# Kernel optimization log

Measured on AMD Instinct MI355X. Metric: run time of the kernel, lower is better.

Reference implementation:

```python
import jax, jax.numpy as jnp
import numpy as np

DIM = 768
H = 6        # pinned by router mask construction (3 logits -> 6 head gates)
HD = DIM // H  # 128
TAU = 5.0

def setup_inputs() -> dict:
    key = jax.random.key(0)
    ks = jax.random.split(key, 10)
    w = 0.02
    return {
        "x": jax.random.normal(ks[0], (4, 2048, DIM), jnp.float32),
        "latency": jax.random.uniform(ks[1], (1,), jnp.float32),
        "qkv_w": jax.random.normal(ks[2], (3 * DIM, DIM), jnp.float32) * w,
        "qkv_b": jax.random.normal(ks[3], (3 * DIM,), jnp.float32) * w,
        "proj_w": jax.random.normal(ks[4], (DIM, DIM), jnp.float32) * w,
        "proj_b": jax.random.normal(ks[5], (DIM,), jnp.float32) * w,
        "router_w": jax.random.normal(ks[6], (3, 1), jnp.float32),
        "router_b": jax.random.normal(ks[7], (3,), jnp.float32),
        # gumbel noise g = -log(Exp(1)), matching -empty.exponential_().log()
        "g1": -jnp.log(jax.random.exponential(ks[8], (3,), jnp.float32)),
        "g2": -jnp.log(jax.random.exponential(ks[9], (3,), jnp.float32)),
    }

def reference(x, latency, qkv_w, qkv_b, proj_w, proj_b, router_w, router_b, g1, g2):
    # router: Linear(1, 3) on scalar latency -> 3 logits
    logits = router_w @ latency + router_b                      # [3]
    # gumbel-sigmoid, tau=5, hard=True with straight-through estimator
    y_soft = jax.nn.sigmoid((logits + g1 - g2) / TAU)           # [3]
    y_hard = (y_soft > 0.5).astype(y_soft.dtype)
    mask3 = y_hard - jax.lax.stop_gradient(y_soft) + y_soft     # [3]
    # first logit gates 4 heads, remaining two gate one head each -> 6 heads
    mask6 = jnp.concatenate([mask3[:1], mask3[:1], mask3[:1], mask3])  # [6]
    maskC = jnp.repeat(mask6, HD)                               # [DIM]

    B, N, C = x.shape
    qkv = jnp.einsum('bnc,oc->bno', x, qkv_w) + qkv_b           # [B,N,3*DIM]
    qkv = qkv.reshape(B, N, 3, H, HD)
    q, k, v = qkv[:, :, 0], qkv[:, :, 1], qkv[:, :, 2]          # [B,N,H,HD]

    scale = HD ** -0.5
    attn = jax.nn.softmax(jnp.einsum('bqhd,bkhd->bhqk', q * scale, k), axis=-1)
    out = jnp.einsum('bhqk,bkhd->bqhd', attn, v).reshape(B, N, C)

    out = out * maskC                                            # gate heads/channels
    return jnp.einsum('bnc,oc->bno', out, proj_w) + proj_b
```

## Files before the change

### kernel.cpp

```cpp
#include <hip/hip_runtime.h>
#include <cstdint>

#define DIM_ 768
#define H_ 6
#define HD_ 128
#define NB_ 4
#define SEQ_ 2048
#define TOK_ (NB_*SEQ_)
#define OUT3_ (3*DIM_)
#define L2E 1.4426950408889634f

typedef __bf16 bf16;
typedef __bf16 bf16x4 __attribute__((ext_vector_type(4)));
typedef __bf16 bf16x8 __attribute__((ext_vector_type(8)));
typedef float f32x4 __attribute__((ext_vector_type(4)));
typedef float f32x16 __attribute__((ext_vector_type(16)));
typedef unsigned int u32;
typedef u32 u32x4 __attribute__((ext_vector_type(4)));

__device__ __forceinline__ void gload16(const void* g, void* lds) {
  __builtin_amdgcn_global_load_lds((const __attribute__((address_space(1))) void*)g,
                                   (__attribute__((address_space(3))) void*)lds,
                                   16, 0, 0);
}

__global__ void convert_kernel(const float* __restrict__ in, bf16* __restrict__ out, int n) {
  int i = (blockIdx.x * 256 + threadIdx.x) * 4;
  if (i >= n) return;
  float4 v = *reinterpret_cast<const float4*>(in + i);
  bf16x4 o = { (bf16)v.x, (bf16)v.y, (bf16)v.z, (bf16)v.w };
  *reinterpret_cast<bf16x4*>(out + i) = o;
}

__global__ void mask_kernel(const float* __restrict__ latency,
                            const float* __restrict__ rw,
                            const float* __restrict__ rb,
                            const float* __restrict__ g1,
                            const float* __restrict__ g2,
                            float* __restrict__ mask6) {
  int i = threadIdx.x;
  if (i < 6) {
    int j = (i < 4) ? 0 : (i - 3);
    float logit = rw[j] * latency[0] + rb[j];
    float z = (logit + g1[j] - g2[j]) / 5.0f;
    float ys = 1.0f / (1.0f + expf(-z));
    float yh = ys > 0.5f ? 1.0f : 0.0f;
    mask6[i] = (yh - ys) + ys;
  }
}


__global__ __launch_bounds__(256)
void qkv_gemm(const bf16* __restrict__ A, const bf16* __restrict__ W,
              const float* __restrict__ bias,
              bf16* __restrict__ q, bf16* __restrict__ k, bf16* __restrict__ vt) {
  __shared__ bf16 As[128 * 32];
  __shared__ bf16 Bs[128 * 32];
  __shared__ bf16 FragS[8192];
  const int tid = threadIdx.x;
  const int l = tid & 63, w = tid >> 6;
  const int lr = l & 15, lg = l >> 4;
  const int wm = w >> 1, wn = w & 1;
  const int tm = blockIdx.y * 128;
  const int on = blockIdx.x * 128;

  f32x4 acc[4][4];
#pragma unroll
  for (int i = 0; i < 4; ++i)
#pragma unroll
    for (int j = 0; j < 4; ++j) acc[i][j] = f32x4{0.f, 0.f, 0.f, 0.f};

  for (int k0 = 0; k0 < DIM_; k0 += 32) {
    __syncthreads();
#pragma unroll
    for (int u = 0; u < 2; ++u) {
      int row = w * 32 + u * 16 + (l >> 2);
      int cb = l & 3;
      gload16(A + (size_t)(tm + row) * DIM_ + k0 + cb * 8, As + (w * 32 + u * 16) * 32);
      gload16(W + (size_t)(on + row) * DIM_ + k0 + cb * 8, Bs + (w * 32 + u * 16) * 32);
    }
    __syncthreads();
    bf16x8 af[4], bfr[4];
#pragma unroll
    for (int i = 0; i < 4; ++i)
      af[i] = *reinterpret_cast<const bf16x8*>(As + (wm * 64 + i * 16 + lr) * 32 + lg * 8);
#pragma unroll
    for (int j = 0; j < 4; ++j)
      bfr[j] = *reinterpret_cast<const bf16x8*>(Bs + (wn * 64 + j * 16 + lr) * 32 + lg * 8);
#pragma unroll
    for (int i = 0; i < 4; ++i)
#pragma unroll
      for (int j = 0; j < 4; ++j)
        acc[i][j] = __builtin_amdgcn_mfma_f32_16x16x32_bf16(af[i], bfr[j], acc[i][j], 0, 0, 0);
  }

  if (on < 2 * DIM_) {
    const int s = on / DIM_;
    const float scale = 0.08838834764831845f * L2E;
    const int n0 = tm & 2047;
    const int bb = tm >> 11;
    const int hh = (on - s * DIM_) >> 7;
    const int bhh = bb * H_ + hh;
    bf16* dstbase = (s == 0) ? q : k;
    for (int pass = 0; pass < 2; ++pass) {
      __syncthreads();
      if (wm == pass) {
#pragma unroll
        for (int i = 0; i < 4; ++i) {
#pragma unroll
          for (int j = 0; j < 4; ++j) {
            int dd = wn * 64 + j * 16 + lr;
            int kc = dd >> 4, hi8 = (dd >> 3) & 1, e = dd & 7;
            float bia = bias[on + dd];
#pragma unroll
            for (int r = 0; r < 4; ++r) {
              int nl = i * 16 + lg * 4 + r;
              float val = acc[i][j][r] + bia;
              if (s == 0) val *= scale;
              FragS[(((nl >> 5) * 8 + kc) << 9) + ((hi8 * 32 + (nl & 31)) << 3) + e] = (bf16)val;
            }
          }
        }
      }
      __syncthreads();
      size_t base = ((size_t)bhh * 64 + (n0 >> 5) + pass * 2) * 4096;
#pragma unroll
      for (int r8 = 0; r8 < 4; ++r8) {
        bf16x8 v8 = *reinterpret_cast<const bf16x8*>(FragS + r8 * 2048 + tid * 8);
        *reinterpret_cast<bf16x8*>(dstbase + base + r8 * 2048 + tid * 8) = v8;
      }
    }
  } else {
    const int hh = (on - 2 * DIM_) >> 7;
    const int bb = tm >> 11, n0 = tm & 2047;
    const int bhh = bb * H_ + hh;
    bf16(*Ts)[136] = reinterpret_cast<bf16(*)[136]>(As);
    for (int wc = 0; wc < 2; ++wc) {
#pragma unroll
      for (int j = 0; j < 4; ++j) {
        __syncthreads();
        if (wn == wc) {
          float bia = bias[on + wc * 64 + j * 16 + lr];
#pragma unroll
          for (int i = 0; i < 4; ++i) {
            bf16x4 pk;
#pragma unroll
            for (int r = 0; r < 4; ++r) pk[r] = (bf16)(acc[i][j][r] + bia);
            *reinterpret_cast<bf16x4*>(&Ts[lr][wm * 64 + i * 16 + lg * 4]) = pk;
          }
        }
        __syncthreads();
        int row = tid >> 4;
        int c8 = (tid & 15) * 8;
        bf16x8 v8 = *reinterpret_cast<const bf16x8*>(&Ts[row][c8]);
        int d = wc * 64 + j * 16 + row;
        int n = n0 + c8;
        size_t idx = (((((size_t)bhh * 32 + (n >> 6)) * 4 + ((n >> 4) & 3)) * 4 + (d >> 5)) << 9) +
                     ((((n >> 3) & 1) * 32 + (d & 31)) << 3);
        *reinterpret_cast<bf16x8*>(vt + idx) = v8;
      }
    }
  }
}

__global__ __launch_bounds__(256)
void proj_gemm(const bf16* __restrict__ A, const bf16* __restrict__ W,
               const float* __restrict__ bias, float* __restrict__ out) {
  __shared__ bf16 As[128 * 32];
  __shared__ bf16 Bs[128 * 32];
  const int tid = threadIdx.x;
  const int l = tid & 63, w = tid >> 6;
  const int lr = l & 15, lg = l >> 4;
  const int wm = w >> 1, wn = w & 1;
  const int tm = blockIdx.y * 128;
  const int on = blockIdx.x * 128;

  f32x4 acc[4][4];
#pragma unroll
  for (int i = 0; i < 4; ++i)
#pragma unroll
    for (int j = 0; j < 4; ++j) acc[i][j] = f32x4{0.f, 0.f, 0.f, 0.f};

  for (int k0 = 0; k0 < DIM_; k0 += 32) {
    __syncthreads();
#pragma unroll
    for (int u = 0; u < 2; ++u) {
      int row = w * 32 + u * 16 + (l >> 2);
      int cb = l & 3;
      gload16(A + (size_t)(tm + row) * DIM_ + k0 + cb * 8, As + (w * 32 + u * 16) * 32);
      gload16(W + (size_t)(on + row) * DIM_ + k0 + cb * 8, Bs + (w * 32 + u * 16) * 32);
    }
    __syncthreads();
    bf16x8 af[4], bfr[4];
#pragma unroll
    for (int i = 0; i < 4; ++i)
      af[i] = *reinterpret_cast<const bf16x8*>(As + (wm * 64 + i * 16 + lr) * 32 + lg * 8);
#pragma unroll
    for (int j = 0; j < 4; ++j)
      bfr[j] = *reinterpret_cast<const bf16x8*>(Bs + (wn * 64 + j * 16 + lr) * 32 + lg * 8);
#pragma unroll
    for (int i = 0; i < 4; ++i)
#pragma unroll
      for (int j = 0; j < 4; ++j)
        acc[i][j] = __builtin_amdgcn_mfma_f32_16x16x32_bf16(af[i], bfr[j], acc[i][j], 0, 0, 0);
  }

#pragma unroll
  for (int i = 0; i < 4; ++i) {
#pragma unroll
    for (int j = 0; j < 4; ++j) {
      int o = on + wn * 64 + j * 16 + lr;
      float bia = bias[o];
#pragma unroll
      for (int r = 0; r < 4; ++r) {
        int t = tm + wm * 64 + i * 16 + lg * 4 + r;
        out[(size_t)t * DIM_ + o] = acc[i][j][r] + bia;
      }
    }
  }
}

__global__ __launch_bounds__(128, 2)
void attn_kernel(const bf16* __restrict__ qf_g, const bf16* __restrict__ kf_g,
                 const bf16* __restrict__ vf_g, const float* __restrict__ mask6,
                 bf16* __restrict__ ab) {
  __shared__ char smem[16640];

  const int tid = threadIdx.x;
  const int l = tid & 63;
  const int w = tid >> 6;
  const int kl = l & 31, hi = l >> 5;
  const int bid = blockIdx.x;
  const int bh = bid % 24;
  const int qt = bid / 24;
  const int h = bh % H_;
  const int b = bh / H_;
  const int q0 = qt * 32;
  const int loff = l * 8;
  const float hm = mask6[h];

  if (hm == 0.0f) {
    bf16x8 z = __builtin_bit_cast(bf16x8, u32x4{0u, 0u, 0u, 0u});
    int row = tid >> 2, c0 = (tid & 3) * 32;
    bf16* dst = ab + ((size_t)b * SEQ_ + q0 + row) * DIM_ + h * HD_ + c0;
#pragma unroll
    for (int u = 0; u < 4; ++u)
      *reinterpret_cast<bf16x8*>(dst + u * 8) = z;
    return;
  }

  float* OM  = (float*)smem;
  float* MLm = (float*)(smem + 16384);
  float* MLl = MLm + 32;

  const bf16* qq = qf_g + (((size_t)bh * 64 + qt) * 8) * 512;
  const bf16* kq = kf_g + (size_t)bh * 262144 + (size_t)w * 32 * 4096;
  const bf16* vq = vf_g + (size_t)bh * 262144 + (size_t)w * 32 * 4096;

  bf16x8 qf[8];
#pragma unroll
  for (int kc = 0; kc < 8; ++kc)
    qf[kc] = *reinterpret_cast<const bf16x8*>(qq + kc * 512 + loff);

  f32x16 oacc[4];
#pragma unroll
  for (int df = 0; df < 4; ++df)
#pragma unroll
    for (int r = 0; r < 16; ++r) oacc[df][r] = 0.f;
  float m_lane = -3.0e38f;
  float lsum = 0.f;

  for (int jj = 0; jj < 32; ++jj) {
    const bf16* kb = kq + (size_t)jj * 4096;
    const bf16* vb = vq + (size_t)jj * 4096;

    f32x16 sacc;
#pragma unroll
    for (int r = 0; r < 16; ++r) sacc[r] = 0.f;
    __builtin_amdgcn_s_setprio(1);
#pragma unroll
    for (int kc = 0; kc < 8; ++kc) {
      bf16x8 kfr = *reinterpret_cast<const bf16x8*>(kb + kc * 512 + loff);
      sacc = __builtin_amdgcn_mfma_f32_32x32x16_bf16(kfr, qf[kc], sacc, 0, 0, 0);
    }
    __builtin_amdgcn_s_setprio(0);

    float t = sacc[0];
#pragma unroll
    for (int r = 1; r < 16; ++r) t = fmaxf(t, sacc[r]);
    t = fmaxf(t, __shfl_xor(t, 32));
    bool need = t > m_lane + 8.0f;
    if (__ballot(need) != 0ull) {
      float nm = fmaxf(m_lane, t);
      float c = exp2f(m_lane - nm);
      m_lane = nm;
      lsum *= c;
#pragma unroll
      for (int r = 0; r < 16; ++r) {
        float cr = __shfl(c, (r & 3) + 8 * (r >> 2) + 4 * hi);
#pragma unroll
        for (int df = 0; df < 4; ++df) oacc[df][r] *= cr;
      }
    }

    u32 pp[8];
#pragma unroll
    for (int m = 0; m < 8; ++m) {
      float e0 = exp2f(sacc[2 * m] - m_lane);
      float e1 = exp2f(sacc[2 * m + 1] - m_lane);
      lsum += e0 + e1;
      union { u32 u; bf16 hh2[2]; } pk;
      pk.hh2[0] = (bf16)e0; pk.hh2[1] = (bf16)e1;
      pp[m] = pk.u;
    }

    u32x4 afv[2];
#pragma unroll
    for (int ks = 0; ks < 2; ++ks) {
#pragma unroll
      for (int i = 0; i < 2; ++i) {
        u32 a = pp[4 * ks + i];
        u32 b2 = pp[4 * ks + 2 + i];
        asm volatile("v_permlane32_swap_b32 %0, %1" : "+v"(a), "+v"(b2));
        afv[ks][i] = a;
        afv[ks][2 + i] = b2;
      }
    }

    __builtin_amdgcn_s_setprio(1);
#pragma unroll
    for (int ks = 0; ks < 2; ++ks) {
      bf16x8 pa = __builtin_bit_cast(bf16x8, afv[ks]);
#pragma unroll
      for (int df = 0; df < 4; ++df) {
        bf16x8 vfr = *reinterpret_cast<const bf16x8*>(vb + (ks * 4 + df) * 512 + loff);
        oacc[df] = __builtin_amdgcn_mfma_f32_32x32x16_bf16(pa, vfr, oacc[df], 0, 0, 0);
      }
    }
    __builtin_amdgcn_s_setprio(0);
  }

  float lt = lsum + __shfl_xor(lsum, 32);

  if (w == 1) {
#pragma unroll
    for (int r = 0; r < 16; ++r) {
      int qloc = (r & 3) + 8 * (r >> 2) + 4 * hi;
#pragma unroll
      for (int df = 0; df < 4; ++df)
        OM[qloc * 128 + df * 32 + kl] = oacc[df][r];
    }
    MLm[kl] = m_lane;
    MLl[kl] = lt;
  }
  __syncthreads();
  if (w == 1) return;

  float m1 = MLm[kl];
  float l1 = MLl[kl];
  float M = fmaxf(m_lane, m1);
  float a0 = exp2f(m_lane - M), a1 = exp2f(m1 - M);
  float L = lt * a0 + l1 * a1;
  float s0 = a0 * hm / L, s1 = a1 * hm / L;

#pragma unroll
  for (int r = 0; r < 16; ++r) {
    int qloc = (r & 3) + 8 * (r >> 2) + 4 * hi;
    float r0 = __shfl(s0, qloc);
    float r1 = __shfl(s1, qloc);
    int n = q0 + qloc;
#pragma unroll
    for (int df = 0; df < 4; ++df) {
      int d = df * 32 + kl;
      float o1 = OM[qloc * 128 + df * 32 + kl];
      ab[((size_t)b * SEQ_ + n) * DIM_ + h * HD_ + d] =
          (bf16)(oacc[df][r] * r0 + o1 * r1);
    }
  }
}

extern "C" void kernel_launch(void* const* d_in, const int* in_sizes, int n_in,
                              void* d_out, int out_size, void* d_ws, size_t ws_size,
                              hipStream_t stream) {
  const float* x        = (const float*)d_in[0];
  const float* latency  = (const float*)d_in[1];
  const float* qkv_w    = (const float*)d_in[2];
  const float* qkv_b    = (const float*)d_in[3];
  const float* proj_w   = (const float*)d_in[4];
  const float* proj_b   = (const float*)d_in[5];
  const float* router_w = (const float*)d_in[6];
  const float* router_b = (const float*)d_in[7];
  const float* g1       = (const float*)d_in[8];
  const float* g2       = (const float*)d_in[9];
  float* out = (float*)d_out;

  const size_t N_X  = (size_t)TOK_ * DIM_;
  const size_t N_WQ = (size_t)OUT3_ * DIM_;
  const size_t N_WP = (size_t)DIM_ * DIM_;
  const size_t N_P  = (size_t)NB_ * H_ * SEQ_ * HD_;

  float* maskp = (float*)d_ws;
  bf16* xb  = (bf16*)((char*)d_ws + 256);
  bf16* wqb = xb + N_X;
  bf16* wpb = wqb + N_WQ;
  bf16* qbf = wpb + N_WP;
  bf16* kbf = qbf + N_P;
  bf16* vtb = kbf + N_P;
  bf16* abf = vtb + N_P;

  size_t need = 256 + 2 * (N_X + N_WQ + N_WP + 4 * N_P);
  if (ws_size < need) return;

  convert_kernel<<<(int)(N_X / 1024), 256, 0, stream>>>(x, xb, (int)N_X);
  convert_kernel<<<(int)(N_WQ / 1024), 256, 0, stream>>>(qkv_w, wqb, (int)N_WQ);
  convert_kernel<<<(int)(N_WP / 1024), 256, 0, stream>>>(proj_w, wpb, (int)N_WP);
  mask_kernel<<<1, 64, 0, stream>>>(latency, router_w, router_b, g1, g2, maskp);

  qkv_gemm<<<dim3(OUT3_ / 128, TOK_ / 128), 256, 0, stream>>>(xb, wqb, qkv_b, qbf, kbf, vtb);
  attn_kernel<<<dim3(24 * (SEQ_ / 32)), 128, 0, stream>>>(qbf, kbf, vtb, maskp, abf);
  proj_gemm<<<dim3(DIM_ / 128, TOK_ / 128), 256, 0, stream>>>(abf, wpb, proj_b, out);
}
```

Baseline: 189.1 us.

## Split attention KV range across four waves with tree merge

The attention block grows from two to four waves, and each wave now processes a quarter of the key/value sequence instead of a half. Partial softmax states are merged in two stages through shared memory: odd waves merge into even waves, then wave 2 into wave 0. The aim is to shorten each wave's serial loop and add parallelism per query tile. The cost is more shared memory, extra barriers and merge work, and possibly fewer resident blocks per CU.

```diff
diff --git a/kernel.cpp b/kernel.cpp
--- a/kernel.cpp
+++ b/kernel.cpp
@@ -220,11 +220,11 @@
   }
 }
 
-__global__ __launch_bounds__(128, 2)
+__global__ __launch_bounds__(256, 4)
 void attn_kernel(const bf16* __restrict__ qf_g, const bf16* __restrict__ kf_g,
                  const bf16* __restrict__ vf_g, const float* __restrict__ mask6,
                  bf16* __restrict__ ab) {
-  __shared__ char smem[16640];
+  __shared__ char smem[33280];
 
   const int tid = threadIdx.x;
   const int l = tid & 63;
@@ -241,21 +241,21 @@
 
   if (hm == 0.0f) {
     bf16x8 z = __builtin_bit_cast(bf16x8, u32x4{0u, 0u, 0u, 0u});
-    int row = tid >> 2, c0 = (tid & 3) * 32;
+    int row = tid >> 3, c0 = (tid & 7) * 16;
     bf16* dst = ab + ((size_t)b * SEQ_ + q0 + row) * DIM_ + h * HD_ + c0;
-#pragma unroll
-    for (int u = 0; u < 4; ++u)
-      *reinterpret_cast<bf16x8*>(dst + u * 8) = z;
+    *reinterpret_cast<bf16x8*>(dst) = z;
+    *reinterpret_cast<bf16x8*>(dst + 8) = z;
     return;
   }
 
-  float* OM  = (float*)smem;
-  float* MLm = (float*)(smem + 16384);
-  float* MLl = MLm + 32;
+  float* OM0 = (float*)smem;
+  float* OM1 = (float*)(smem + 16384);
+  float* MLm = (float*)(smem + 32768);
+  float* MLl = MLm + 64;
 
   const bf16* qq = qf_g + (((size_t)bh * 64 + qt) * 8) * 512;
-  const bf16* kq = kf_g + (size_t)bh * 262144 + (size_t)w * 32 * 4096;
-  const bf16* vq = vf_g + (size_t)bh * 262144 + (size_t)w * 32 * 4096;
+  const bf16* kq = kf_g + (size_t)bh * 262144;
+  const bf16* vq = vf_g + (size_t)bh * 262144;
 
   bf16x8 qf[8];
 #pragma unroll
@@ -270,9 +270,9 @@
   float m_lane = -3.0e38f;
   float lsum = 0.f;
 
-  for (int jj = 0; jj < 32; ++jj) {
-    const bf16* kb = kq + (size_t)jj * 4096;
-    const bf16* vb = vq + (size_t)jj * 4096;
+  for (int it = 0; it < 16; ++it) {
+    const bf16* kb = kq + (size_t)(w * 16 + it) * 4096;
+    const bf16* vb = vq + (size_t)(w * 16 + it) * 4096;
 
     f32x16 sacc;
 #pragma unroll
@@ -342,7 +342,8 @@
 
   float lt = lsum + __shfl_xor(lsum, 32);
 
-  if (w == 1) {
+  if (w & 1) {
+    float* OM = (w >> 1) ? OM1 : OM0;
 #pragma unroll
     for (int r = 0; r < 16; ++r) {
       int qloc = (r & 3) + 8 * (r >> 2) + 4 * hi;
@@ -350,11 +351,42 @@
       for (int df = 0; df < 4; ++df)
         OM[qloc * 128 + df * 32 + kl] = oacc[df][r];
     }
+    MLm[(w >> 1) * 32 + kl] = m_lane;
+    MLl[(w >> 1) * 32 + kl] = lt;
+  }
+  __syncthreads();
+  if (!(w & 1)) {
+    float* OM = (w >> 1) ? OM1 : OM0;
+    float m1 = MLm[(w >> 1) * 32 + kl];
+    float l1 = MLl[(w >> 1) * 32 + kl];
+    float M = fmaxf(m_lane, m1);
+    float a0 = exp2f(m_lane - M), a1 = exp2f(m1 - M);
+    lt = lt * a0 + l1 * a1;
+    m_lane = M;
+#pragma unroll
+    for (int r = 0; r < 16; ++r) {
+      int qloc = (r & 3) + 8 * (r >> 2) + 4 * hi;
+      float r0 = __shfl(a0, qloc);
+      float r1 = __shfl(a1, qloc);
+#pragma unroll
+      for (int df = 0; df < 4; ++df)
+        oacc[df][r] = oacc[df][r] * r0 + OM[qloc * 128 + df * 32 + kl] * r1;
+    }
+  }
+  __syncthreads();
+  if (w == 2) {
+#pragma unroll
+    for (int r = 0; r < 16; ++r) {
+      int qloc = (r & 3) + 8 * (r >> 2) + 4 * hi;
+#pragma unroll
+      for (int df = 0; df < 4; ++df)
+        OM0[qloc * 128 + df * 32 + kl] = oacc[df][r];
+    }
     MLm[kl] = m_lane;
     MLl[kl] = lt;
   }
   __syncthreads();
-  if (w == 1) return;
+  if (w != 0) return;
 
   float m1 = MLm[kl];
   float l1 = MLl[kl];
@@ -372,7 +404,7 @@
 #pragma unroll
     for (int df = 0; df < 4; ++df) {
       int d = df * 32 + kl;
-      float o1 = OM[qloc * 128 + df * 32 + kl];
+      float o1 = OM0[qloc * 128 + df * 32 + kl];
       ab[((size_t)b * SEQ_ + n) * DIM_ + h * HD_ + d] =
           (bf16)(oacc[df][r] * r0 + o1 * r1);
     }
@@ -417,6 +449,6 @@
   mask_kernel<<<1, 64, 0, stream>>>(latency, router_w, router_b, g1, g2, maskp);
 
   qkv_gemm<<<dim3(OUT3_ / 128, TOK_ / 128), 256, 0, stream>>>(xb, wqb, qkv_b, qbf, kbf, vtb);
-  attn_kernel<<<dim3(24 * (SEQ_ / 32)), 128, 0, stream>>>(qbf, kbf, vtb, maskp, abf);
+  attn_kernel<<<dim3(24 * (SEQ_ / 32)), 256, 0, stream>>>(qbf, kbf, vtb, maskp, abf);
   proj_gemm<<<dim3(DIM_ / 128, TOK_ / 128), 256, 0, stream>>>(abf, wpb, proj_b, out);
 }
```

Measured after the change: 260.2 us. +37.6%, slower.
